# Performance work log

Hardware: AMD Instinct MI355X
Metric: run time of the kernel (lower is better)

The kernel has to match this reference:

```python
import jax, jax.numpy as jnp
jax.config.update("jax_enable_x64", True)
import numpy as np
from jax.scipy.linalg import expm as _expm

B, C = 64, 2048


def setup_inputs() -> dict:
    key = jax.random.key(0)
    k1, _ = jax.random.split(key)
    A = jax.random.normal(k1, (B, C, 13, 13), dtype=jnp.float32) * 0.1
    MTMs = jnp.einsum('bcij,bcik->bcjk', A, A)  # PSD normal-equation matrix M^T M
    T0 = jnp.eye(4, dtype=jnp.float32).at[2, 3].set(1.0)  # identity pose, t_z = 1
    Ts = jnp.broadcast_to(T0, (B, C, 4, 4))
    return {"MTMs": MTMs, "Ts": Ts}


def _POfT(T):
    # T: [B,C,4,4] -> P: [B,C,13,7] mapping (rx,ry,rz,tx,ty,tz,1) -> d(TBar)
    z = jnp.zeros(T.shape[:2], T.dtype)
    o = jnp.ones_like(z)
    def rot_rows(i):
        a, b, c = T[..., i, 0], T[..., i, 1], T[..., i, 2]
        return [jnp.stack([z, -c, b, z, z, z, a], -1),
                jnp.stack([c, z, -a, z, z, z, b], -1),
                jnp.stack([-b, a, z, z, z, z, c], -1)]
    rows = rot_rows(0) + rot_rows(1) + rot_rows(2)
    rows.append(jnp.stack([z, z, z, z, z, z, o], -1))
    for i in range(3):
        rows.append(jnp.stack([z, z, z, T[..., i, 0], T[..., i, 1], T[..., i, 2], T[..., i, 3]], -1))
    return jnp.stack(rows, axis=-2)


def _diffT(v):
    # v: [B,C,>=6,1] -> se(3) matrix [B,C,4,4]
    z = jnp.zeros(v.shape[:2], v.dtype)
    vx, vy, vz, tx, ty, tz = (v[..., i, 0] for i in range(6))
    rows = [jnp.stack([z, -vz, vy, tx], -1),
            jnp.stack([vz, z, -vx, ty], -1),
            jnp.stack([-vy, vx, z, tz], -1),
            jnp.stack([z, z, z, z], -1)]
    return jnp.stack(rows, axis=-2)


_expm_b = jax.vmap(jax.vmap(_expm))  # batched 4x4 matrix exponential


def _inv(M):
    # regularized inverse as in the original `inv`
    reg = 1e-5 * (1.0 + jnp.max(M, axis=(-2, -1), keepdims=True))
    eye = jnp.eye(M.shape[-1], dtype=M.dtype)
    return jnp.linalg.inv(M + eye * reg)


def _refine_step(MtM, T):
    # one pnpRefineMtM iteration (lendata=None branch)
    P = _POfT(T)                                    # [B,C,13,7]
    Q = jnp.einsum('bcji,bcjk,bckl->bcil', P, MtM, P)  # P^T MtM P : [B,C,7,7]
    regR = jnp.full(Q.shape[:2], 10.0, Q.dtype)
    regT = 1e-8 * jnp.maximum(Q[..., 3, 3] + Q[..., 4, 4] + Q[..., 5, 5],
                              jnp.ones_like(regR))
    d = jnp.stack([regR, regR, regR, regT, regT, regT], -1)  # [B,C,6]
    Omega = Q[..., 0:6, 0:6] + jnp.eye(6, dtype=Q.dtype) * d[..., None, :]
    v = -jnp.matmul(_inv(Omega), Q[..., 0:6, 6:7])  # [B,C,6,1]
    Tnew = jnp.matmul(T, _expm_b(_diffT(v)))        # boxplus: T @ expm(hat(v))
    Omega_out = Omega / (Tnew[..., 2:3, 3:4] ** 2 + 1e-8)
    return Tnew, Omega_out


def reference(MTMs, Ts):
    MtM = MTMs.astype(jnp.float64)
    T = Ts.astype(jnp.float64)
    Omega = None
    for _ in range(5):  # unrolled 5 Gauss-Newton iterations, as in call()
        T, Omega = _refine_step(MtM, T)
    return T, Omega
```

## Files before the change

kernel.cpp:

```cpp
#include <hip/hip_runtime.h>
#include <math.h>

#define NPROB (64 * 2048)

__host__ __device__ constexpr int TRI(int i, int j) { return i * 13 - i * (i - 1) / 2 + (j - i); }
__host__ __device__ constexpr int OI6(int i, int j) { return i * 6 - i * (i - 1) / 2 + (j - i); }
__host__ __device__ constexpr int QI(int i, int j)  { return i * 7 - i * (i - 1) / 2 + (j - i); }

struct PE { int r, a, b, s; };
__device__ constexpr int PLEN[7] = {6, 6, 6, 3, 3, 3, 13};
__device__ constexpr PE PAT[7][13] = {
    {{1,0,2,1},{2,0,1,-1},{4,1,2,1},{5,1,1,-1},{7,2,2,1},{8,2,1,-1}},
    {{0,0,2,-1},{2,0,0,1},{3,1,2,-1},{5,1,0,1},{6,2,2,-1},{8,2,0,1}},
    {{0,0,1,1},{1,0,0,-1},{3,1,1,1},{4,1,0,-1},{6,2,1,1},{7,2,0,-1}},
    {{10,0,0,1},{11,1,0,1},{12,2,0,1}},
    {{10,0,1,1},{11,1,1,1},{12,2,1,1}},
    {{10,0,2,1},{11,1,2,1},{12,2,2,1}},
    {{0,0,0,1},{1,0,1,1},{2,0,2,1},{3,1,0,1},{4,1,1,1},{5,1,2,1},
     {6,2,0,1},{7,2,1,1},{8,2,2,1},{9,3,0,1},{10,0,3,1},{11,1,3,1},{12,2,3,1}},
};

__global__ __launch_bounds__(256) void gn5_kernel(const float* __restrict__ Mg,
                                                  const float* __restrict__ Tg,
                                                  float* __restrict__ outg) {
    const int tid  = threadIdx.x;
    const int lane = tid & 63;
    const int wv   = tid >> 6;
    const long long prob = (long long)blockIdx.x * 256 + tid;

    __shared__ __align__(16) float buf[64 * 169];
    float mreg[91];

    #pragma unroll 1
    for (int w = 0; w < 4; ++w) {
        const long long c0 = (long long)blockIdx.x * 256 + (long long)w * 64;
        const float4* src = (const float4*)(Mg + c0 * 169);
        float4* dst = (float4*)buf;
        #pragma unroll 1
        for (int i = tid; i < (64 * 169) / 4; i += 256) dst[i] = src[i];
        __syncthreads();
        if (wv == w) {
            #pragma unroll
            for (int i = 0; i < 13; ++i)
                #pragma unroll
                for (int j = i; j < 13; ++j)
                    mreg[TRI(i, j)] = buf[lane * 169 + i * 13 + j];
        }
        __syncthreads();
    }

    double t[3][4];
    {
        const float* tp = Tg + prob * 16;
        #pragma unroll
        for (int i = 0; i < 3; ++i)
            #pragma unroll
            for (int j = 0; j < 4; ++j)
                t[i][j] = (double)tp[i * 4 + j];
    }

    double q[28];

    #pragma unroll 1
    for (int it = 0; it < 5; ++it) {
        float tf[3][4];
        #pragma unroll
        for (int i = 0; i < 3; ++i)
            #pragma unroll
            for (int j = 0; j < 4; ++j)
                tf[i][j] = (float)t[i][j];

        #pragma unroll
        for (int l = 0; l < 7; ++l) {
            float y[13];
            #pragma unroll
            for (int r = 0; r < 13; ++r) y[r] = 0.0f;
            #pragma unroll
            for (int e = 0; e < 13; ++e) {
                if (e < PLEN[l]) {
                    const PE pe = PAT[l][e];
                    const float tt = (pe.a == 3) ? 1.0f : tf[pe.a][pe.b];
                    const float cf = (pe.s > 0) ? tt : -tt;
                    const int c = pe.r;
                    #pragma unroll
                    for (int r = 0; r < 13; ++r)
                        y[r] += cf * mreg[(r <= c) ? TRI(r, c) : TRI(c, r)];
                }
            }
            #pragma unroll
            for (int k = 0; k <= l; ++k) {
                double acc = 0.0;
                #pragma unroll
                for (int e = 0; e < 13; ++e) {
                    if (e < PLEN[k]) {
                        const PE pe = PAT[k][e];
                        const double tt = (pe.a == 3) ? 1.0 : t[pe.a][pe.b];
                        const double coef = (pe.s > 0) ? tt : -tt;
                        acc += coef * (double)y[pe.r];
                    }
                }
                q[QI(k, l)] = acc;
            }
        }

        const double trQ  = q[QI(3, 3)] + q[QI(4, 4)] + q[QI(5, 5)];
        const double regT = 1e-8 * fmax(trQ, 1.0);
        q[QI(0, 0)] += 10.0;
        q[QI(1, 1)] += 10.0;
        q[QI(2, 2)] += 10.0;
        q[QI(3, 3)] += regT;
        q[QI(4, 4)] += regT;
        q[QI(5, 5)] += regT;

        const double a0 = fmax(q[QI(0,0)], q[QI(0,1)]);
        const double a1 = fmax(q[QI(0,2)], q[QI(0,3)]);
        const double a2 = fmax(q[QI(0,4)], q[QI(0,5)]);
        const double a3 = fmax(q[QI(1,1)], q[QI(1,2)]);
        const double a4 = fmax(q[QI(1,3)], q[QI(1,4)]);
        const double a5 = fmax(q[QI(1,5)], q[QI(2,2)]);
        const double a6 = fmax(q[QI(2,3)], q[QI(2,4)]);
        const double a7 = fmax(q[QI(2,5)], q[QI(3,3)]);
        const double a8 = fmax(q[QI(3,4)], q[QI(3,5)]);
        const double a9 = fmax(q[QI(4,4)], q[QI(4,5)]);
        const double b0 = fmax(a0, a1);
        const double b1 = fmax(a2, a3);
        const double b2 = fmax(a4, a5);
        const double b3 = fmax(a6, a7);
        const double b4 = fmax(fmax(a8, a9), q[QI(5,5)]);
        const double mx = fmax(fmax(b0, b1), fmax(fmax(b2, b3), b4));
        const double reg2 = 1e-5 * (1.0 + mx);

        if (it == 4) {
            double* st = (double*)buf;
            #pragma unroll
            for (int k = 0; k < 6; ++k)
                #pragma unroll
                for (int l = k; l < 6; ++l)
                    st[(long long)tid * 21 + OI6(k, l)] = q[QI(k, l)];
        }

        #pragma unroll
        for (int k = 0; k < 6; ++k) q[QI(k, k)] += reg2;

        #pragma unroll
        for (int k = 0; k < 6; ++k) {
            const double inv = 1.0 / q[QI(k, k)];
            q[QI(k, k)] = inv;
            #pragma unroll
            for (int i = k + 1; i < 6; ++i) {
                const double f = q[QI(k, i)] * inv;
                #pragma unroll
                for (int j = i; j < 7; ++j) q[QI(i, j)] -= f * q[QI(k, j)];
            }
        }
        double x[6];
        #pragma unroll
        for (int i = 5; i >= 0; --i) {
            double s = q[QI(i, 6)];
            #pragma unroll
            for (int j = i + 1; j < 6; ++j) s -= q[QI(i, j)] * x[j];
            x[i] = s * q[QI(i, i)];
        }
        const double wx = -x[0], wy = -x[1], wz = -x[2];
        const double ux = -x[3], uy = -x[4], uz = -x[5];

        const double tsq = wx * wx + wy * wy + wz * wz;
        double A, B, Cc;
        if (tsq < 0.25) {
            A  = 1.0 + tsq * (-1.0/6 + tsq * (1.0/120 + tsq * (-1.0/5040 + tsq * (1.0/362880
                 + tsq * (-1.0/39916800.0 + tsq * (1.0/6227020800.0 + tsq * (-1.0/1307674368000.0)))))));
            B  = 0.5 + tsq * (-1.0/24 + tsq * (1.0/720 + tsq * (-1.0/40320 + tsq * (1.0/3628800
                 + tsq * (-1.0/479001600.0 + tsq * (1.0/87178291200.0 + tsq * (-1.0/20922789888000.0)))))));
            Cc = 1.0/6 + tsq * (-1.0/120 + tsq * (1.0/5040 + tsq * (-1.0/362880 + tsq * (1.0/39916800.0
                 + tsq * (-1.0/6227020800.0 + tsq * (1.0/1307674368000.0 + tsq * (-1.0/355687428096000.0)))))));
        } else {
            const double th = sqrt(tsq);
            const double s = sin(th), c = cos(th);
            A  = s / th;
            B  = (1.0 - c) / tsq;
            Cc = (th - s) / (tsq * th);
        }
        const double K2xx = wx * wx - tsq, K2yy = wy * wy - tsq, K2zz = wz * wz - tsq;
        const double K2xy = wx * wy, K2xz = wx * wz, K2yz = wy * wz;
        double R[3][3];
        R[0][0] = 1.0 + B * K2xx;      R[0][1] = -A * wz + B * K2xy;  R[0][2] =  A * wy + B * K2xz;
        R[1][0] =  A * wz + B * K2xy;  R[1][1] = 1.0 + B * K2yy;      R[1][2] = -A * wx + B * K2yz;
        R[2][0] = -A * wy + B * K2xz;  R[2][1] =  A * wx + B * K2yz;  R[2][2] = 1.0 + B * K2zz;
        const double V00 = 1.0 + Cc * K2xx,      V01 = -B * wz + Cc * K2xy, V02 =  B * wy + Cc * K2xz;
        const double V10 =  B * wz + Cc * K2xy,  V11 = 1.0 + Cc * K2yy,     V12 = -B * wx + Cc * K2yz;
        const double V20 = -B * wy + Cc * K2xz,  V21 =  B * wx + Cc * K2yz, V22 = 1.0 + Cc * K2zz;
        const double ex = V00 * ux + V01 * uy + V02 * uz;
        const double ey = V10 * ux + V11 * uy + V12 * uz;
        const double ez = V20 * ux + V21 * uy + V22 * uz;

        #pragma unroll
        for (int i = 0; i < 3; ++i) {
            const double a0_ = t[i][0], a1_ = t[i][1], a2_ = t[i][2], a3_ = t[i][3];
            t[i][0] = a0_ * R[0][0] + a1_ * R[1][0] + a2_ * R[2][0];
            t[i][1] = a0_ * R[0][1] + a1_ * R[1][1] + a2_ * R[2][1];
            t[i][2] = a0_ * R[0][2] + a1_ * R[1][2] + a2_ * R[2][2];
            t[i][3] = a0_ * ex + a1_ * ey + a2_ * ez + a3_;
        }
    }

    {
        float* to = outg + prob * 16;
        #pragma unroll
        for (int i = 0; i < 3; ++i)
            #pragma unroll
            for (int j = 0; j < 4; ++j)
                to[i * 4 + j] = (float)t[i][j];
        to[12] = 0.0f; to[13] = 0.0f; to[14] = 0.0f; to[15] = 1.0f;

        const double invden = 1.0 / (t[2][3] * t[2][3] + 1e-8);
        const double* st = (const double*)buf;
        float* oo = outg + (long long)NPROB * 16 + prob * 36;
        #pragma unroll
        for (int k = 0; k < 6; ++k)
            #pragma unroll
            for (int l = 0; l < 6; ++l)
                oo[k * 6 + l] = (float)(st[(long long)tid * 21 + ((k <= l) ? OI6(k, l) : OI6(l, k))] * invden);
    }
}

extern "C" void kernel_launch(void* const* d_in, const int* in_sizes, int n_in,
                              void* d_out, int out_size, void* d_ws, size_t ws_size,
                              hipStream_t stream) {
    const float* Mg = (const float*)d_in[0];
    const float* Tg = (const float*)d_in[1];
    float* out = (float*)d_out;
    (void)in_sizes; (void)n_in; (void)out_size; (void)d_ws; (void)ws_size;

    const int threads = 256;
    const int blocks = NPROB / threads;
    gn5_kernel<<<blocks, threads, 0, stream>>>(Mg, Tg, out);
}
```

Measured before the change: 167.4 us.

## Split each problem across two waves for Q assembly with LDS exchange

Each pose problem is now handled by a pair of wavefronts. One builds Q columns 0,2,4,5 into shared memory and the other builds columns 1,3,6, then does the regularised solve and exponential update and broadcasts the new pose back via LDS. The grid doubles to raise the number of resident waves and split the Q-building work. In exchange it adds two block barriers per iteration, LDS traffic, and leaves half the waves idle during the serial solve.

```diff
diff --git a/kernel.cpp b/kernel.cpp
--- a/kernel.cpp
+++ b/kernel.cpp
@@ -20,31 +20,74 @@
      {6,2,0,1},{7,2,1,1},{8,2,2,1},{9,3,0,1},{10,0,3,1},{11,1,3,1},{12,2,3,1}},
 };
 
+template <int L, typename F>
+__device__ __forceinline__ void build_col(const float mreg[91], const float tf[3][4],
+                                          const double t[3][4], F emit) {
+    float y[13];
+    #pragma unroll
+    for (int r = 0; r < 13; ++r) y[r] = 0.0f;
+    #pragma unroll
+    for (int e = 0; e < 13; ++e) {
+        if (e < PLEN[L]) {
+            const PE pe = PAT[L][e];
+            const float tt = (pe.a == 3) ? 1.0f : tf[pe.a][pe.b];
+            const float cf = (pe.s > 0) ? tt : -tt;
+            const int c = pe.r;
+            #pragma unroll
+            for (int r = 0; r < 13; ++r)
+                y[r] += cf * mreg[(r <= c) ? TRI(r, c) : TRI(c, r)];
+        }
+    }
+    #pragma unroll
+    for (int k = 0; k <= L; ++k) {
+        double acc = 0.0;
+        #pragma unroll
+        for (int e = 0; e < 13; ++e) {
+            if (e < PLEN[k]) {
+                const PE pe = PAT[k][e];
+                const double tt = (pe.a == 3) ? 1.0 : t[pe.a][pe.b];
+                const double coef = (pe.s > 0) ? tt : -tt;
+                acc += coef * (double)y[pe.r];
+            }
+        }
+        emit(k, acc);
+    }
+}
+
 __global__ __launch_bounds__(256) void gn5_kernel(const float* __restrict__ Mg,
                                                   const float* __restrict__ Tg,
                                                   float* __restrict__ outg) {
     const int tid  = threadIdx.x;
     const int lane = tid & 63;
     const int wv   = tid >> 6;
-    const long long prob = (long long)blockIdx.x * 256 + tid;
-
-    __shared__ __align__(16) float buf[64 * 169];
+    const int pair = wv >> 1;
+    const int role = wv & 1;
+    const long long prob = (long long)blockIdx.x * 128 + (long long)pair * 64 + lane;
+
+    __shared__ __align__(16) char smem[28672];
+    float* buf = (float*)smem;
+    double* smemd = (double*)smem;
+    double* qx    = smemd + pair * 1792 + lane * 15;
+    double* tb    = smemd + pair * 1792 + 960 + lane * 13;
+    double* stash = smemd + pair * 1792 + lane * 21;
+
     float mreg[91];
 
     #pragma unroll 1
-    for (int w = 0; w < 4; ++w) {
-        const long long c0 = (long long)blockIdx.x * 256 + (long long)w * 64;
-        const float4* src = (const float4*)(Mg + c0 * 169);
+    for (int c = 0; c < 4; ++c) {
+        const long long p0 = (long long)blockIdx.x * 128 + c * 32;
+        const float4* src = (const float4*)(Mg + p0 * 169);
         float4* dst = (float4*)buf;
         #pragma unroll 1
-        for (int i = tid; i < (64 * 169) / 4; i += 256) dst[i] = src[i];
+        for (int i = tid; i < (32 * 169) / 4; i += 256) dst[i] = src[i];
         __syncthreads();
-        if (wv == w) {
+        if (pair == (c >> 1) && (lane >> 5) == (c & 1)) {
+            const int lidx = lane & 31;
             #pragma unroll
             for (int i = 0; i < 13; ++i)
                 #pragma unroll
                 for (int j = i; j < 13; ++j)
-                    mreg[TRI(i, j)] = buf[lane * 169 + i * 13 + j];
+                    mreg[TRI(i, j)] = buf[lidx * 169 + i * 13 + j];
         }
         __syncthreads();
     }
@@ -70,140 +113,148 @@
             for (int j = 0; j < 4; ++j)
                 tf[i][j] = (float)t[i][j];
 
-        #pragma unroll
-        for (int l = 0; l < 7; ++l) {
-            float y[13];
-            #pragma unroll
-            for (int r = 0; r < 13; ++r) y[r] = 0.0f;
-            #pragma unroll
-            for (int e = 0; e < 13; ++e) {
-                if (e < PLEN[l]) {
-                    const PE pe = PAT[l][e];
-                    const float tt = (pe.a == 3) ? 1.0f : tf[pe.a][pe.b];
-                    const float cf = (pe.s > 0) ? tt : -tt;
-                    const int c = pe.r;
-                    #pragma unroll
-                    for (int r = 0; r < 13; ++r)
-                        y[r] += cf * mreg[(r <= c) ? TRI(r, c) : TRI(c, r)];
+        if (role == 1) {
+            build_col<0>(mreg, tf, t, [&](int k, double a) { qx[0 + k] = a; });
+            build_col<2>(mreg, tf, t, [&](int k, double a) { qx[1 + k] = a; });
+            build_col<4>(mreg, tf, t, [&](int k, double a) { qx[4 + k] = a; });
+            build_col<5>(mreg, tf, t, [&](int k, double a) { qx[9 + k] = a; });
+        } else {
+            build_col<1>(mreg, tf, t, [&](int k, double a) { q[QI(k, 1)] = a; });
+            build_col<3>(mreg, tf, t, [&](int k, double a) { q[QI(k, 3)] = a; });
+            build_col<6>(mreg, tf, t, [&](int k, double a) { q[QI(k, 6)] = a; });
+        }
+
+        __syncthreads();
+
+        if (role == 0) {
+            q[QI(0, 0)] = qx[0];
+            #pragma unroll
+            for (int k = 0; k <= 2; ++k) q[QI(k, 2)] = qx[1 + k];
+            #pragma unroll
+            for (int k = 0; k <= 4; ++k) q[QI(k, 4)] = qx[4 + k];
+            #pragma unroll
+            for (int k = 0; k <= 5; ++k) q[QI(k, 5)] = qx[9 + k];
+
+            const double trQ  = q[QI(3, 3)] + q[QI(4, 4)] + q[QI(5, 5)];
+            const double regT = 1e-8 * fmax(trQ, 1.0);
+            q[QI(0, 0)] += 10.0;
+            q[QI(1, 1)] += 10.0;
+            q[QI(2, 2)] += 10.0;
+            q[QI(3, 3)] += regT;
+            q[QI(4, 4)] += regT;
+            q[QI(5, 5)] += regT;
+
+            const double a0 = fmax(q[QI(0,0)], q[QI(0,1)]);
+            const double a1 = fmax(q[QI(0,2)], q[QI(0,3)]);
+            const double a2 = fmax(q[QI(0,4)], q[QI(0,5)]);
+            const double a3 = fmax(q[QI(1,1)], q[QI(1,2)]);
+            const double a4 = fmax(q[QI(1,3)], q[QI(1,4)]);
+            const double a5 = fmax(q[QI(1,5)], q[QI(2,2)]);
+            const double a6 = fmax(q[QI(2,3)], q[QI(2,4)]);
+            const double a7 = fmax(q[QI(2,5)], q[QI(3,3)]);
+            const double a8 = fmax(q[QI(3,4)], q[QI(3,5)]);
+            const double a9 = fmax(q[QI(4,4)], q[QI(4,5)]);
+            const double b0 = fmax(a0, a1);
+            const double b1 = fmax(a2, a3);
+            const double b2 = fmax(a4, a5);
+            const double b3 = fmax(a6, a7);
+            const double b4 = fmax(fmax(a8, a9), q[QI(5,5)]);
+            const double mx = fmax(fmax(b0, b1), fmax(fmax(b2, b3), b4));
+            const double reg2 = 1e-5 * (1.0 + mx);
+
+            if (it == 4) {
+                #pragma unroll
+                for (int k = 0; k < 6; ++k)
+                    #pragma unroll
+                    for (int l = k; l < 6; ++l)
+                        stash[OI6(k, l)] = q[QI(k, l)];
+            }
+
+            #pragma unroll
+            for (int k = 0; k < 6; ++k) q[QI(k, k)] += reg2;
+
+            #pragma unroll
+            for (int k = 0; k < 6; ++k) {
+                const double inv = 1.0 / q[QI(k, k)];
+                q[QI(k, k)] = inv;
+                #pragma unroll
+                for (int i = k + 1; i < 6; ++i) {
+                    const double f = q[QI(k, i)] * inv;
+                    #pragma unroll
+                    for (int j = i; j < 7; ++j) q[QI(i, j)] -= f * q[QI(k, j)];
                 }
             }
-            #pragma unroll
-            for (int k = 0; k <= l; ++k) {
-                double acc = 0.0;
-                #pragma unroll
-                for (int e = 0; e < 13; ++e) {
-                    if (e < PLEN[k]) {
-                        const PE pe = PAT[k][e];
-                        const double tt = (pe.a == 3) ? 1.0 : t[pe.a][pe.b];
-                        const double coef = (pe.s > 0) ? tt : -tt;
-                        acc += coef * (double)y[pe.r];
-                    }
-                }
-                q[QI(k, l)] = acc;
-            }
-        }
-
-        const double trQ  = q[QI(3, 3)] + q[QI(4, 4)] + q[QI(5, 5)];
-        const double regT = 1e-8 * fmax(trQ, 1.0);
-        q[QI(0, 0)] += 10.0;
-        q[QI(1, 1)] += 10.0;
-        q[QI(2, 2)] += 10.0;
-        q[QI(3, 3)] += regT;
-        q[QI(4, 4)] += regT;
-        q[QI(5, 5)] += regT;
-
-        const double a0 = fmax(q[QI(0,0)], q[QI(0,1)]);
-        const double a1 = fmax(q[QI(0,2)], q[QI(0,3)]);
-        const double a2 = fmax(q[QI(0,4)], q[QI(0,5)]);
-        const double a3 = fmax(q[QI(1,1)], q[QI(1,2)]);
-        const double a4 = fmax(q[QI(1,3)], q[QI(1,4)]);
-        const double a5 = fmax(q[QI(1,5)], q[QI(2,2)]);
-        const double a6 = fmax(q[QI(2,3)], q[QI(2,4)]);
-        const double a7 = fmax(q[QI(2,5)], q[QI(3,3)]);
-        const double a8 = fmax(q[QI(3,4)], q[QI(3,5)]);
-        const double a9 = fmax(q[QI(4,4)], q[QI(4,5)]);
-        const double b0 = fmax(a0, a1);
-        const double b1 = fmax(a2, a3);
-        const double b2 = fmax(a4, a5);
-        const double b3 = fmax(a6, a7);
-        const double b4 = fmax(fmax(a8, a9), q[QI(5,5)]);
-        const double mx = fmax(fmax(b0, b1), fmax(fmax(b2, b3), b4));
-        const double reg2 = 1e-5 * (1.0 + mx);
-
-        if (it == 4) {
-            double* st = (double*)buf;
-            #pragma unroll
-            for (int k = 0; k < 6; ++k)
-                #pragma unroll
-                for (int l = k; l < 6; ++l)
-                    st[(long long)tid * 21 + OI6(k, l)] = q[QI(k, l)];
-        }
-
-        #pragma unroll
-        for (int k = 0; k < 6; ++k) q[QI(k, k)] += reg2;
-
-        #pragma unroll
-        for (int k = 0; k < 6; ++k) {
-            const double inv = 1.0 / q[QI(k, k)];
-            q[QI(k, k)] = inv;
-            #pragma unroll
-            for (int i = k + 1; i < 6; ++i) {
-                const double f = q[QI(k, i)] * inv;
-                #pragma unroll
-                for (int j = i; j < 7; ++j) q[QI(i, j)] -= f * q[QI(k, j)];
-            }
-        }
-        double x[6];
-        #pragma unroll
-        for (int i = 5; i >= 0; --i) {
-            double s = q[QI(i, 6)];
-            #pragma unroll
-            for (int j = i + 1; j < 6; ++j) s -= q[QI(i, j)] * x[j];
-            x[i] = s * q[QI(i, i)];
-        }
-        const double wx = -x[0], wy = -x[1], wz = -x[2];
-        const double ux = -x[3], uy = -x[4], uz = -x[5];
-
-        const double tsq = wx * wx + wy * wy + wz * wz;
-        double A, B, Cc;
-        if (tsq < 0.25) {
-            A  = 1.0 + tsq * (-1.0/6 + tsq * (1.0/120 + tsq * (-1.0/5040 + tsq * (1.0/362880
-                 + tsq * (-1.0/39916800.0 + tsq * (1.0/6227020800.0 + tsq * (-1.0/1307674368000.0)))))));
-            B  = 0.5 + tsq * (-1.0/24 + tsq * (1.0/720 + tsq * (-1.0/40320 + tsq * (1.0/3628800
-                 + tsq * (-1.0/479001600.0 + tsq * (1.0/87178291200.0 + tsq * (-1.0/20922789888000.0)))))));
-            Cc = 1.0/6 + tsq * (-1.0/120 + tsq * (1.0/5040 + tsq * (-1.0/362880 + tsq * (1.0/39916800.0
-                 + tsq * (-1.0/6227020800.0 + tsq * (1.0/1307674368000.0 + tsq * (-1.0/355687428096000.0)))))));
-        } else {
-            const double th = sqrt(tsq);
-            const double s = sin(th), c = cos(th);
-            A  = s / th;
-            B  = (1.0 - c) / tsq;
-            Cc = (th - s) / (tsq * th);
-        }
-        const double K2xx = wx * wx - tsq, K2yy = wy * wy - tsq, K2zz = wz * wz - tsq;
-        const double K2xy = wx * wy, K2xz = wx * wz, K2yz = wy * wz;
-        double R[3][3];
-        R[0][0] = 1.0 + B * K2xx;      R[0][1] = -A * wz + B * K2xy;  R[0][2] =  A * wy + B * K2xz;
-        R[1][0] =  A * wz + B * K2xy;  R[1][1] = 1.0 + B * K2yy;      R[1][2] = -A * wx + B * K2yz;
-        R[2][0] = -A * wy + B * K2xz;  R[2][1] =  A * wx + B * K2yz;  R[2][2] = 1.0 + B * K2zz;
-        const double V00 = 1.0 + Cc * K2xx,      V01 = -B * wz + Cc * K2xy, V02 =  B * wy + Cc * K2xz;
-        const double V10 =  B * wz + Cc * K2xy,  V11 = 1.0 + Cc * K2yy,     V12 = -B * wx + Cc * K2yz;
-        const double V20 = -B * wy + Cc * K2xz,  V21 =  B * wx + Cc * K2yz, V22 = 1.0 + Cc * K2zz;
-        const double ex = V00 * ux + V01 * uy + V02 * uz;
-        const double ey = V10 * ux + V11 * uy + V12 * uz;
-        const double ez = V20 * ux + V21 * uy + V22 * uz;
-
-        #pragma unroll
-        for (int i = 0; i < 3; ++i) {
-            const double a0_ = t[i][0], a1_ = t[i][1], a2_ = t[i][2], a3_ = t[i][3];
-            t[i][0] = a0_ * R[0][0] + a1_ * R[1][0] + a2_ * R[2][0];
-            t[i][1] = a0_ * R[0][1] + a1_ * R[1][1] + a2_ * R[2][1];
-            t[i][2] = a0_ * R[0][2] + a1_ * R[1][2] + a2_ * R[2][2];
-            t[i][3] = a0_ * ex + a1_ * ey + a2_ * ez + a3_;
-        }
-    }
-
-    {
+            double x[6];
+            #pragma unroll
+            for (int i = 5; i >= 0; --i) {
+                double s = q[QI(i, 6)];
+                #pragma unroll
+                for (int j = i + 1; j < 6; ++j) s -= q[QI(i, j)] * x[j];
+                x[i] = s * q[QI(i, i)];
+            }
+            const double wx = -x[0], wy = -x[1], wz = -x[2];
+            const double ux = -x[3], uy = -x[4], uz = -x[5];
+
+            const double tsq = wx * wx + wy * wy + wz * wz;
+            double A, B, Cc;
+            if (tsq < 0.25) {
+                A  = 1.0 + tsq * (-1.0/6 + tsq * (1.0/120 + tsq * (-1.0/5040 + tsq * (1.0/362880
+                     + tsq * (-1.0/39916800.0 + tsq * (1.0/6227020800.0 + tsq * (-1.0/1307674368000.0)))))));
+                B  = 0.5 + tsq * (-1.0/24 + tsq * (1.0/720 + tsq * (-1.0/40320 + tsq * (1.0/3628800
+                     + tsq * (-1.0/479001600.0 + tsq * (1.0/87178291200.0 + tsq * (-1.0/20922789888000.0)))))));
+                Cc = 1.0/6 + tsq * (-1.0/120 + tsq * (1.0/5040 + tsq * (-1.0/362880 + tsq * (1.0/39916800.0
+                     + tsq * (-1.0/6227020800.0 + tsq * (1.0/1307674368000.0 + tsq * (-1.0/355687428096000.0)))))));
+            } else {
+                const double th = sqrt(tsq);
+                const double s = sin(th), c = cos(th);
+                A  = s / th;
+                B  = (1.0 - c) / tsq;
+                Cc = (th - s) / (tsq * th);
+            }
+            const double K2xx = wx * wx - tsq, K2yy = wy * wy - tsq, K2zz = wz * wz - tsq;
+            const double K2xy = wx * wy, K2xz = wx * wz, K2yz = wy * wz;
+            double R[3][3];
+            R[0][0] = 1.0 + B * K2xx;      R[0][1] = -A * wz + B * K2xy;  R[0][2] =  A * wy + B * K2xz;
+            R[1][0] =  A * wz + B * K2xy;  R[1][1] = 1.0 + B * K2yy;      R[1][2] = -A * wx + B * K2yz;
+            R[2][0] = -A * wy + B * K2xz;  R[2][1] =  A * wx + B * K2yz;  R[2][2] = 1.0 + B * K2zz;
+            const double V00 = 1.0 + Cc * K2xx,      V01 = -B * wz + Cc * K2xy, V02 =  B * wy + Cc * K2xz;
+            const double V10 =  B * wz + Cc * K2xy,  V11 = 1.0 + Cc * K2yy,     V12 = -B * wx + Cc * K2yz;
+            const double V20 = -B * wy + Cc * K2xz,  V21 =  B * wx + Cc * K2yz, V22 = 1.0 + Cc * K2zz;
+            const double ex = V00 * ux + V01 * uy + V02 * uz;
+            const double ey = V10 * ux + V11 * uy + V12 * uz;
+            const double ez = V20 * ux + V21 * uy + V22 * uz;
+
+            #pragma unroll
+            for (int i = 0; i < 3; ++i) {
+                const double c0_ = t[i][0], c1_ = t[i][1], c2_ = t[i][2], c3_ = t[i][3];
+                t[i][0] = c0_ * R[0][0] + c1_ * R[1][0] + c2_ * R[2][0];
+                t[i][1] = c0_ * R[0][1] + c1_ * R[1][1] + c2_ * R[2][1];
+                t[i][2] = c0_ * R[0][2] + c1_ * R[1][2] + c2_ * R[2][2];
+                t[i][3] = c0_ * ex + c1_ * ey + c2_ * ez + c3_;
+            }
+
+            if (it < 4) {
+                #pragma unroll
+                for (int i = 0; i < 3; ++i)
+                    #pragma unroll
+                    for (int j = 0; j < 4; ++j)
+                        tb[i * 4 + j] = t[i][j];
+            }
+        }
+
+        if (it < 4) {
+            __syncthreads();
+            if (role == 1) {
+                #pragma unroll
+                for (int i = 0; i < 3; ++i)
+                    #pragma unroll
+                    for (int j = 0; j < 4; ++j)
+                        t[i][j] = tb[i * 4 + j];
+            }
+        }
+    }
+
+    if (role == 0) {
         float* to = outg + prob * 16;
         #pragma unroll
         for (int i = 0; i < 3; ++i)
@@ -213,13 +264,12 @@
         to[12] = 0.0f; to[13] = 0.0f; to[14] = 0.0f; to[15] = 1.0f;
 
         const double invden = 1.0 / (t[2][3] * t[2][3] + 1e-8);
-        const double* st = (const double*)buf;
         float* oo = outg + (long long)NPROB * 16 + prob * 36;
         #pragma unroll
         for (int k = 0; k < 6; ++k)
             #pragma unroll
             for (int l = 0; l < 6; ++l)
-                oo[k * 6 + l] = (float)(st[(long long)tid * 21 + ((k <= l) ? OI6(k, l) : OI6(l, k))] * invden);
+                oo[k * 6 + l] = (float)(stash[(k <= l) ? OI6(k, l) : OI6(l, k)] * invden);
     }
 }
 
@@ -232,6 +282,6 @@
     (void)in_sizes; (void)n_in; (void)out_size; (void)d_ws; (void)ws_size;
 
     const int threads = 256;
-    const int blocks = NPROB / threads;
+    const int blocks = NPROB / 128;
     gn5_kernel<<<blocks, threads, 0, stream>>>(Mg, Tg, out);
 }
```

Measured after the change: 226.3 us. 1.35x slower.
